# Optimization experiments

Measured on AMD Instinct MI355X. Metric: run time of the kernel, lower is better.

Reference implementation:

```python
import jax, jax.numpy as jnp
import numpy as np

B, T, N, C, K = 32, 16, 512, 128, 2


def setup_inputs() -> dict:
    key = jax.random.key(0)
    k1, k2, k3 = jax.random.split(key, 3)
    x = jax.random.normal(k1, (B, T, N, C), dtype=jnp.float32)
    adj = jax.random.uniform(k2, (B, N, N), dtype=jnp.float32)
    lambdas = jnp.ones((K,), dtype=jnp.float32)           # raw lambda params (init 1.0)
    thetas = jax.random.uniform(k3, (K, C, C), dtype=jnp.float32)  # torch.rand init
    return {"x": x, "adj": adj, "lambdas": lambdas, "thetas": thetas}


def _akgcn_layer(x, adj, lam_raw, theta):
    # x: [B,T,N,C], adj: [B,N,N]
    lam = 1.0 + jax.nn.relu(lam_raw)  # actual lambda
    h = jnp.einsum('btnc,cd->btnd', x, theta)
    eye = jnp.eye(adj.shape[-1], dtype=adj.dtype)
    v = ((2.0 * lam - 2.0) / lam) * eye + (2.0 / lam) * adj   # [B,N,N]
    v = v / jnp.sum(v, axis=-1, keepdims=True)                 # row-normalize
    out = jnp.einsum('bnm,btmd->btnd', v, h)                   # vectorized over T
    return jax.nn.relu(out)


def reference(x, adj, lambdas, thetas):
    hid = x
    for k in range(K):  # small fixed layer count
        hid = _akgcn_layer(hid, adj, lambdas[k], thetas[k])
    return jax.nn.relu(x) + jax.nn.sigmoid(hid)
```

## Files before the change

### kernel.cpp

```cpp
#include <hip/hip_runtime.h>
#include <hip/hip_bf16.h>

#define BB 32
#define TT 16
#define NNODE 512
#define CC 128

typedef __attribute__((ext_vector_type(8))) short bf16x8;
typedef __attribute__((ext_vector_type(4))) short short4_t;
typedef __attribute__((ext_vector_type(4))) float f32x4;

__device__ __forceinline__ short f2bf(float f) {
    __hip_bfloat16 h = __float2bfloat16(f);
    return *reinterpret_cast<short*>(&h);
}

#define GLD16(g, l)                                                          \
    __builtin_amdgcn_global_load_lds(                                        \
        (const __attribute__((address_space(1))) unsigned int*)(g),          \
        (__attribute__((address_space(3))) unsigned int*)(l), 16, 0, 0)

__global__ void prep_adj_kernel(const float* __restrict__ adj,
                                const float* __restrict__ lambdas, int layer0,
                                short* __restrict__ Abf0,
                                short* __restrict__ Abf1) {
    int gid = blockIdx.x * blockDim.x + threadIdx.x;
    int row = gid >> 6;
    int lane = gid & 63;
    int n = row & (NNODE - 1);
    const float* r = adj + (long)row * NNODE;
    float4 f0 = *(const float4*)(r + lane * 4);
    float4 f1 = *(const float4*)(r + 256 + lane * 4);
    float s = f0.x + f0.y + f0.z + f0.w + f1.x + f1.y + f1.z + f1.w;
#pragma unroll
    for (int o = 32; o; o >>= 1) s += __shfl_xor(s, o, 64);
    float base[8] = {f0.x, f0.y, f0.z, f0.w, f1.x, f1.y, f1.z, f1.w};
    int d0 = n - lane * 4;
    int d1 = n - 256 - lane * 4;
#pragma unroll
    for (int l = 0; l < 2; ++l) {
        short* dst = l ? Abf1 : Abf0;
        if (dst == nullptr) continue;
        float lamm1 = fmaxf(lambdas[layer0 + l], 0.f);
        float inv = 1.f / (s + lamm1);
        float v[8];
#pragma unroll
        for (int j = 0; j < 8; ++j) v[j] = base[j] * inv;
        if (d0 >= 0 && d0 < 4) v[d0] += lamm1 * inv;
        if (d1 >= 0 && d1 < 4) v[4 + d1] += lamm1 * inv;
        short* o = dst + (long)row * NNODE;
        short4_t s0 = {f2bf(v[0]), f2bf(v[1]), f2bf(v[2]), f2bf(v[3])};
        short4_t s1 = {f2bf(v[4]), f2bf(v[5]), f2bf(v[6]), f2bf(v[7])};
        *(short4_t*)(o + lane * 4) = s0;
        *(short4_t*)(o + 256 + lane * 4) = s1;
    }
}

__global__ void prep_theta_kernel(const float* __restrict__ thetas,
                                  short* __restrict__ thT) {
    int idx = blockIdx.x * 256 + threadIdx.x;
    int l = idx >> 14;
    int r = idx & 16383;
    int i = r >> 7, k = r & (CC - 1);
    thT[l * CC * CC + i * CC + k] = f2bf(thetas[l * CC * CC + k * CC + i]);
}

__global__ __launch_bounds__(256) void gemm_theta_mfma(
    const float* __restrict__ X, const short* __restrict__ thT,
    short* __restrict__ Ht) {
    __shared__ short Bs[128][136];
    const int t = threadIdx.x;
    const long rowBase = (long)blockIdx.x * 128;
    const int w = t >> 6, ln = t & 63;
    const int lm = ln & 15, q = ln >> 4;
    const int wy = w >> 1, wx = w & 1;

    {
        int row = t >> 1, half = (t & 1) * 64;
        const short* src = thT + row * CC + half;
#pragma unroll
        for (int j = 0; j < 8; ++j)
            *(bf16x8*)(&Bs[row][half + j * 8]) = *(const bf16x8*)(src + j * 8);
    }
    __syncthreads();

    f32x4 acc[4][4] = {};
    const float* Xr = X + (rowBase + wy * 64 + lm) * CC;
#pragma unroll
    for (int k0 = 0; k0 < CC; k0 += 32) {
        bf16x8 a[4], b[4];
#pragma unroll
        for (int i = 0; i < 4; ++i) {
            const float* p = Xr + i * 16 * CC + k0 + q * 8;
            float4 g0 = *(const float4*)(p);
            float4 g1 = *(const float4*)(p + 4);
            bf16x8 av;
            av[0] = f2bf(g0.x); av[1] = f2bf(g0.y);
            av[2] = f2bf(g0.z); av[3] = f2bf(g0.w);
            av[4] = f2bf(g1.x); av[5] = f2bf(g1.y);
            av[6] = f2bf(g1.z); av[7] = f2bf(g1.w);
            a[i] = av;
        }
#pragma unroll
        for (int j = 0; j < 4; ++j)
            b[j] = *(const bf16x8*)(&Bs[wx * 64 + j * 16 + lm][k0 + q * 8]);
#pragma unroll
        for (int i = 0; i < 4; ++i)
#pragma unroll
            for (int j = 0; j < 4; ++j)
                acc[i][j] = __builtin_amdgcn_mfma_f32_16x16x32_bf16(
                    a[i], b[j], acc[i][j], 0, 0, 0);
    }

    const long bt = rowBase >> 9;
    const int mBase = (int)(rowBase & (NNODE - 1));
    short* Hb = Ht + bt * (long)(NNODE * CC);
#pragma unroll
    for (int i = 0; i < 4; ++i) {
        int m = mBase + wy * 64 + i * 16 + q * 4;
#pragma unroll
        for (int j = 0; j < 4; ++j) {
            int c = wx * 64 + j * 16 + lm;
            f32x4 v = acc[i][j];
            short4_t sv = {f2bf(v[0]), f2bf(v[1]), f2bf(v[2]), f2bf(v[3])};
            *(short4_t*)(&Hb[(long)c * NNODE + m]) = sv;
        }
    }
}

__global__ __launch_bounds__(256) void gemm_agg_theta(
    const short* __restrict__ Abf, const short* __restrict__ Ht1,
    const short* __restrict__ thT2, short* __restrict__ Ht2) {
    __shared__ short sh[17408];
    const int t = threadIdx.x;
    const int bid = blockIdx.x;
    const int wid = (bid & 7) * 256 + (bid >> 3);
    const int bt = wid >> 2;
    const int n0 = (wid & 3) * 128;
    const short* Ab = Abf + (long)(bt >> 4) * NNODE * NNODE + (long)n0 * NNODE;
    const short* Hb = Ht1 + (long)bt * NNODE * CC;
    const int w = t >> 6, ln = t & 63;
    const int lm = ln & 15, q = ln >> 4;
    const int wy = w >> 1, wx = w & 1;

    f32x4 acc[4][4] = {};

    const int rr = w * 32 + (ln >> 2);
    const int kc = (ln & 3) * 8;
    const short* ga = Ab + (long)rr * NNODE + kc;
    const short* gb = Hb + (long)rr * NNODE + kc;
    const int lofs = w * 1024 + ln * 8;

    GLD16(ga, sh + lofs);
    GLD16(ga + 16 * NNODE, sh + lofs + 512);
    GLD16(gb, sh + 8192 + lofs);
    GLD16(gb + 16 * NNODE, sh + 8192 + lofs + 512);
    __syncthreads();
    int sel = 0;
    for (int k0 = 0; k0 < NNODE; k0 += 32) {
        if (k0 + 32 < NNODE) {
            const int no = (sel ^ 1) * 4096 + lofs;
            GLD16(ga + k0 + 32, sh + no);
            GLD16(ga + k0 + 32 + 16 * NNODE, sh + no + 512);
            GLD16(gb + k0 + 32, sh + 8192 + no);
            GLD16(gb + k0 + 32 + 16 * NNODE, sh + 8192 + no + 512);
        }
        const short* Ac = sh + sel * 4096;
        const short* Bc = sh + 8192 + sel * 4096;
        bf16x8 a[4], b[4];
#pragma unroll
        for (int i = 0; i < 4; ++i)
            a[i] = *(const bf16x8*)(Ac + (wy * 64 + i * 16 + lm) * 32 + q * 8);
#pragma unroll
        for (int j = 0; j < 4; ++j)
            b[j] = *(const bf16x8*)(Bc + (wx * 64 + j * 16 + lm) * 32 + q * 8);
#pragma unroll
        for (int i = 0; i < 4; ++i)
#pragma unroll
            for (int j = 0; j < 4; ++j)
                acc[i][j] = __builtin_amdgcn_mfma_f32_16x16x32_bf16(
                    a[i], b[j], acc[i][j], 0, 0, 0);
        __syncthreads();
        sel ^= 1;
    }

    short(*Ts)[136] = (short(*)[136])sh;
#pragma unroll
    for (int i = 0; i < 4; ++i)
#pragma unroll
        for (int j = 0; j < 4; ++j)
#pragma unroll
            for (int r2 = 0; r2 < 4; ++r2)
                Ts[wy * 64 + i * 16 + q * 4 + r2][wx * 64 + j * 16 + lm] =
                    f2bf(fmaxf(acc[i][j][r2], 0.f));
    __syncthreads();

    f32x4 acc2[4][4] = {};
#pragma unroll
    for (int c0 = 0; c0 < CC; c0 += 32) {
        bf16x8 a[4], b[4];
#pragma unroll
        for (int i = 0; i < 4; ++i)
            a[i] = *(const bf16x8*)(&Ts[wy * 64 + i * 16 + lm][c0 + q * 8]);
#pragma unroll
        for (int j = 0; j < 4; ++j)
            b[j] = *(const bf16x8*)(thT2 + (wx * 64 + j * 16 + lm) * CC + c0 +
                                    q * 8);
#pragma unroll
        for (int i = 0; i < 4; ++i)
#pragma unroll
            for (int j = 0; j < 4; ++j)
                acc2[i][j] = __builtin_amdgcn_mfma_f32_16x16x32_bf16(
                    a[i], b[j], acc2[i][j], 0, 0, 0);
    }

    short* Hb2 = Ht2 + (long)bt * NNODE * CC;
#pragma unroll
    for (int i = 0; i < 4; ++i) {
        int m = n0 + wy * 64 + i * 16 + q * 4;
#pragma unroll
        for (int j = 0; j < 4; ++j) {
            int c = wx * 64 + j * 16 + lm;
            f32x4 v = acc2[i][j];
            short4_t sv = {f2bf(v[0]), f2bf(v[1]), f2bf(v[2]), f2bf(v[3])};
            *(short4_t*)(&Hb2[(long)c * NNODE + m]) = sv;
        }
    }
}

__global__ __launch_bounds__(256) void gemm_agg_mfma(
    const short* __restrict__ Abf, const short* __restrict__ Ht,
    const float* __restrict__ x, float* __restrict__ Out) {
    __shared__ short sh[16384];
    const int t = threadIdx.x;
    const int bid = blockIdx.x;
    const int wid = (bid & 7) * 256 + (bid >> 3);
    const int bt = wid >> 2;
    const int n0 = (wid & 3) * 128;
    const short* Ab = Abf + (long)(bt >> 4) * NNODE * NNODE + (long)n0 * NNODE;
    const short* Hb = Ht + (long)bt * NNODE * CC;
    const int w = t >> 6, ln = t & 63;
    const int lm = ln & 15, q = ln >> 4;
    const int wy = w >> 1, wx = w & 1;

    f32x4 acc[4][4] = {};

    const int rr = w * 32 + (ln >> 2);
    const int kc = (ln & 3) * 8;
    const short* ga = Ab + (long)rr * NNODE + kc;
    const short* gb = Hb + (long)rr * NNODE + kc;
    const int lofs = w * 1024 + ln * 8;

    GLD16(ga, sh + lofs);
    GLD16(ga + 16 * NNODE, sh + lofs + 512);
    GLD16(gb, sh + 8192 + lofs);
    GLD16(gb + 16 * NNODE, sh + 8192 + lofs + 512);
    __syncthreads();
    int sel = 0;
    for (int k0 = 0; k0 < NNODE; k0 += 32) {
        if (k0 + 32 < NNODE) {
            const int no = (sel ^ 1) * 4096 + lofs;
            GLD16(ga + k0 + 32, sh + no);
            GLD16(ga + k0 + 32 + 16 * NNODE, sh + no + 512);
            GLD16(gb + k0 + 32, sh + 8192 + no);
            GLD16(gb + k0 + 32 + 16 * NNODE, sh + 8192 + no + 512);
        }
        const short* Ac = sh + sel * 4096;
        const short* Bc = sh + 8192 + sel * 4096;
        bf16x8 a[4], b[4];
#pragma unroll
        for (int i = 0; i < 4; ++i)
            a[i] = *(const bf16x8*)(Ac + (wy * 64 + i * 16 + lm) * 32 + q * 8);
#pragma unroll
        for (int j = 0; j < 4; ++j)
            b[j] = *(const bf16x8*)(Bc + (wx * 64 + j * 16 + lm) * 32 + q * 8);
#pragma unroll
        for (int i = 0; i < 4; ++i)
#pragma unroll
            for (int j = 0; j < 4; ++j)
                acc[i][j] = __builtin_amdgcn_mfma_f32_16x16x32_bf16(
                    a[i], b[j], acc[i][j], 0, 0, 0);
        __syncthreads();
        sel ^= 1;
    }

    const long obase = (long)bt * NNODE * CC;
#pragma unroll
    for (int i = 0; i < 4; ++i) {
        int n = n0 + wy * 64 + i * 16 + q * 4;
#pragma unroll
        for (int j = 0; j < 4; ++j) {
            int c = wx * 64 + j * 16 + lm;
#pragma unroll
            for (int r2 = 0; r2 < 4; ++r2) {
                long idx = obase + (long)(n + r2) * CC + c;
                float v = fmaxf(acc[i][j][r2], 0.f);
                Out[idx] = fmaxf(x[idx], 0.f) + 1.f / (1.f + __expf(-v));
            }
        }
    }
}

extern "C" void kernel_launch(void* const* d_in, const int* in_sizes, int n_in,
                              void* d_out, int out_size, void* d_ws,
                              size_t ws_size, hipStream_t stream) {
    const float* x = (const float*)d_in[0];
    const float* adj = (const float*)d_in[1];
    const float* lambdas = (const float*)d_in[2];
    const float* thetas = (const float*)d_in[3];
    float* out = (float*)d_out;

    const long abf_elems = (long)BB * NNODE * NNODE;
    const long ht_elems = (long)BB * TT * NNODE * CC;
    const bool two =
        ws_size >= (size_t)(2 * abf_elems + ht_elems + 2 * CC * CC) * 2;

    short* Abf0 = (short*)d_ws;
    short* Abf1 = two ? Abf0 + abf_elems : Abf0;
    short* Ht2 = Abf1 + abf_elems;
    short* thT0 = Ht2 + ht_elems;
    short* thT1 = thT0 + CC * CC;
    short* Ht1 = (short*)out;

    dim3 blk(256);

    if (two) {
        prep_adj_kernel<<<4096, blk, 0, stream>>>(adj, lambdas, 0, Abf0, Abf1);
        prep_theta_kernel<<<128, blk, 0, stream>>>(thetas, thT0);
        gemm_theta_mfma<<<2048, blk, 0, stream>>>(x, thT0, Ht1);
        gemm_agg_theta<<<2048, blk, 0, stream>>>(Abf0, Ht1, thT1, Ht2);
        gemm_agg_mfma<<<2048, blk, 0, stream>>>(Abf1, Ht2, x, out);
    } else {
        prep_adj_kernel<<<4096, blk, 0, stream>>>(adj, lambdas, 0, Abf0,
                                                  nullptr);
        prep_theta_kernel<<<128, blk, 0, stream>>>(thetas, thT0);
        gemm_theta_mfma<<<2048, blk, 0, stream>>>(x, thT0, Ht1);
        gemm_agg_theta<<<2048, blk, 0, stream>>>(Abf0, Ht1, thT1, Ht2);
        prep_adj_kernel<<<4096, blk, 0, stream>>>(adj, lambdas, 1, Abf0,
                                                  nullptr);
        gemm_agg_mfma<<<2048, blk, 0, stream>>>(Abf0, Ht2, x, out);
    }
}
```

Measured before the change: 504.0 us.

## Replace double-buffered LDS pipeline with single-buffer loads and 2D grid

Drops the double-buffered LDS prefetch in both aggregation GEMMs and uses a single buffer with a sync before and after each tile load. It also replaces the XCD-swizzled 1D block index with a plain 2D grid. In the theta stage, theta is now staged through LDS via global_load_lds instead of being read straight from global memory. This simplifies the code and lowers LDS use, but it gives up the overlap of loads with MFMA and the L2 locality the swizzle provided.

```diff
diff --git a/kernel.cpp b/kernel.cpp
--- a/kernel.cpp
+++ b/kernel.cpp
@@ -131,12 +131,12 @@
 __global__ __launch_bounds__(256) void gemm_agg_theta(
     const short* __restrict__ Abf, const short* __restrict__ Ht1,
     const short* __restrict__ thT2, short* __restrict__ Ht2) {
-    __shared__ short sh[17408];
+    __shared__ short As[128 * 32];
+    __shared__ short Bs[128 * 32];
+    __shared__ short Ts[128][136];
     const int t = threadIdx.x;
-    const int bid = blockIdx.x;
-    const int wid = (bid & 7) * 256 + (bid >> 3);
-    const int bt = wid >> 2;
-    const int n0 = (wid & 3) * 128;
+    const int bt = blockIdx.y;
+    const int n0 = blockIdx.x * 128;
     const short* Ab = Abf + (long)(bt >> 4) * NNODE * NNODE + (long)n0 * NNODE;
     const short* Hb = Ht1 + (long)bt * NNODE * CC;
     const int w = t >> 6, ln = t & 63;
@@ -147,44 +147,34 @@
 
     const int rr = w * 32 + (ln >> 2);
     const int kc = (ln & 3) * 8;
-    const short* ga = Ab + (long)rr * NNODE + kc;
-    const short* gb = Hb + (long)rr * NNODE + kc;
-    const int lofs = w * 1024 + ln * 8;
-
-    GLD16(ga, sh + lofs);
-    GLD16(ga + 16 * NNODE, sh + lofs + 512);
-    GLD16(gb, sh + 8192 + lofs);
-    GLD16(gb + 16 * NNODE, sh + 8192 + lofs + 512);
-    __syncthreads();
-    int sel = 0;
+    short* ldsA = As + w * 1024 + ln * 8;
+    short* ldsB = Bs + w * 1024 + ln * 8;
+
     for (int k0 = 0; k0 < NNODE; k0 += 32) {
-        if (k0 + 32 < NNODE) {
-            const int no = (sel ^ 1) * 4096 + lofs;
-            GLD16(ga + k0 + 32, sh + no);
-            GLD16(ga + k0 + 32 + 16 * NNODE, sh + no + 512);
-            GLD16(gb + k0 + 32, sh + 8192 + no);
-            GLD16(gb + k0 + 32 + 16 * NNODE, sh + 8192 + no + 512);
-        }
-        const short* Ac = sh + sel * 4096;
-        const short* Bc = sh + 8192 + sel * 4096;
+        __syncthreads();
+        const short* ga = Ab + (long)rr * NNODE + k0 + kc;
+        const short* gb = Hb + (long)rr * NNODE + k0 + kc;
+        GLD16(ga, ldsA);
+        GLD16(ga + 16 * NNODE, ldsA + 512);
+        GLD16(gb, ldsB);
+        GLD16(gb + 16 * NNODE, ldsB + 512);
+        __syncthreads();
+
         bf16x8 a[4], b[4];
 #pragma unroll
         for (int i = 0; i < 4; ++i)
-            a[i] = *(const bf16x8*)(Ac + (wy * 64 + i * 16 + lm) * 32 + q * 8);
-#pragma unroll
-        for (int j = 0; j < 4; ++j)
-            b[j] = *(const bf16x8*)(Bc + (wx * 64 + j * 16 + lm) * 32 + q * 8);
+            a[i] = *(const bf16x8*)(&As[(wy * 64 + i * 16 + lm) * 32 + q * 8]);
+#pragma unroll
+        for (int j = 0; j < 4; ++j)
+            b[j] = *(const bf16x8*)(&Bs[(wx * 64 + j * 16 + lm) * 32 + q * 8]);
 #pragma unroll
         for (int i = 0; i < 4; ++i)
 #pragma unroll
             for (int j = 0; j < 4; ++j)
                 acc[i][j] = __builtin_amdgcn_mfma_f32_16x16x32_bf16(
                     a[i], b[j], acc[i][j], 0, 0, 0);
-        __syncthreads();
-        sel ^= 1;
-    }
-
-    short(*Ts)[136] = (short(*)[136])sh;
+    }
+
 #pragma unroll
     for (int i = 0; i < 4; ++i)
 #pragma unroll
@@ -193,19 +183,22 @@
             for (int r2 = 0; r2 < 4; ++r2)
                 Ts[wy * 64 + i * 16 + q * 4 + r2][wx * 64 + j * 16 + lm] =
                     f2bf(fmaxf(acc[i][j][r2], 0.f));
-    __syncthreads();
 
     f32x4 acc2[4][4] = {};
-#pragma unroll
     for (int c0 = 0; c0 < CC; c0 += 32) {
+        __syncthreads();
+        const short* gb = thT2 + rr * CC + c0 + kc;
+        GLD16(gb, ldsB);
+        GLD16(gb + 16 * CC, ldsB + 512);
+        __syncthreads();
+
         bf16x8 a[4], b[4];
 #pragma unroll
         for (int i = 0; i < 4; ++i)
             a[i] = *(const bf16x8*)(&Ts[wy * 64 + i * 16 + lm][c0 + q * 8]);
 #pragma unroll
         for (int j = 0; j < 4; ++j)
-            b[j] = *(const bf16x8*)(thT2 + (wx * 64 + j * 16 + lm) * CC + c0 +
-                                    q * 8);
+            b[j] = *(const bf16x8*)(&Bs[(wx * 64 + j * 16 + lm) * 32 + q * 8]);
 #pragma unroll
         for (int i = 0; i < 4; ++i)
 #pragma unroll
@@ -231,12 +224,11 @@
 __global__ __launch_bounds__(256) void gemm_agg_mfma(
     const short* __restrict__ Abf, const short* __restrict__ Ht,
     const float* __restrict__ x, float* __restrict__ Out) {
-    __shared__ short sh[16384];
+    __shared__ short As[128 * 32];
+    __shared__ short Bs[128 * 32];
     const int t = threadIdx.x;
-    const int bid = blockIdx.x;
-    const int wid = (bid & 7) * 256 + (bid >> 3);
-    const int bt = wid >> 2;
-    const int n0 = (wid & 3) * 128;
+    const int bt = blockIdx.y;
+    const int n0 = blockIdx.x * 128;
     const short* Ab = Abf + (long)(bt >> 4) * NNODE * NNODE + (long)n0 * NNODE;
     const short* Hb = Ht + (long)bt * NNODE * CC;
     const int w = t >> 6, ln = t & 63;
@@ -247,41 +239,32 @@
 
     const int rr = w * 32 + (ln >> 2);
     const int kc = (ln & 3) * 8;
-    const short* ga = Ab + (long)rr * NNODE + kc;
-    const short* gb = Hb + (long)rr * NNODE + kc;
-    const int lofs = w * 1024 + ln * 8;
-
-    GLD16(ga, sh + lofs);
-    GLD16(ga + 16 * NNODE, sh + lofs + 512);
-    GLD16(gb, sh + 8192 + lofs);
-    GLD16(gb + 16 * NNODE, sh + 8192 + lofs + 512);
-    __syncthreads();
-    int sel = 0;
+    short* ldsA = As + w * 1024 + ln * 8;
+    short* ldsB = Bs + w * 1024 + ln * 8;
+
     for (int k0 = 0; k0 < NNODE; k0 += 32) {
-        if (k0 + 32 < NNODE) {
-            const int no = (sel ^ 1) * 4096 + lofs;
-            GLD16(ga + k0 + 32, sh + no);
-            GLD16(ga + k0 + 32 + 16 * NNODE, sh + no + 512);
-            GLD16(gb + k0 + 32, sh + 8192 + no);
-            GLD16(gb + k0 + 32 + 16 * NNODE, sh + 8192 + no + 512);
-        }
-        const short* Ac = sh + sel * 4096;
-        const short* Bc = sh + 8192 + sel * 4096;
+        __syncthreads();
+        const short* ga = Ab + (long)rr * NNODE + k0 + kc;
+        const short* gb = Hb + (long)rr * NNODE + k0 + kc;
+        GLD16(ga, ldsA);
+        GLD16(ga + 16 * NNODE, ldsA + 512);
+        GLD16(gb, ldsB);
+        GLD16(gb + 16 * NNODE, ldsB + 512);
+        __syncthreads();
+
         bf16x8 a[4], b[4];
 #pragma unroll
         for (int i = 0; i < 4; ++i)
-            a[i] = *(const bf16x8*)(Ac + (wy * 64 + i * 16 + lm) * 32 + q * 8);
-#pragma unroll
-        for (int j = 0; j < 4; ++j)
-            b[j] = *(const bf16x8*)(Bc + (wx * 64 + j * 16 + lm) * 32 + q * 8);
+            a[i] = *(const bf16x8*)(&As[(wy * 64 + i * 16 + lm) * 32 + q * 8]);
+#pragma unroll
+        for (int j = 0; j < 4; ++j)
+            b[j] = *(const bf16x8*)(&Bs[(wx * 64 + j * 16 + lm) * 32 + q * 8]);
 #pragma unroll
         for (int i = 0; i < 4; ++i)
 #pragma unroll
             for (int j = 0; j < 4; ++j)
                 acc[i][j] = __builtin_amdgcn_mfma_f32_16x16x32_bf16(
                     a[i], b[j], acc[i][j], 0, 0, 0);
-        __syncthreads();
-        sel ^= 1;
     }
 
     const long obase = (long)bt * NNODE * CC;
@@ -323,21 +306,22 @@
     short* Ht1 = (short*)out;
 
     dim3 blk(256);
+    dim3 g_agg(NNODE / 128, BB * TT);
 
     if (two) {
         prep_adj_kernel<<<4096, blk, 0, stream>>>(adj, lambdas, 0, Abf0, Abf1);
         prep_theta_kernel<<<128, blk, 0, stream>>>(thetas, thT0);
         gemm_theta_mfma<<<2048, blk, 0, stream>>>(x, thT0, Ht1);
-        gemm_agg_theta<<<2048, blk, 0, stream>>>(Abf0, Ht1, thT1, Ht2);
-        gemm_agg_mfma<<<2048, blk, 0, stream>>>(Abf1, Ht2, x, out);
+        gemm_agg_theta<<<g_agg, blk, 0, stream>>>(Abf0, Ht1, thT1, Ht2);
+        gemm_agg_mfma<<<g_agg, blk, 0, stream>>>(Abf1, Ht2, x, out);
     } else {
         prep_adj_kernel<<<4096, blk, 0, stream>>>(adj, lambdas, 0, Abf0,
                                                   nullptr);
         prep_theta_kernel<<<128, blk, 0, stream>>>(thetas, thT0);
         gemm_theta_mfma<<<2048, blk, 0, stream>>>(x, thT0, Ht1);
-        gemm_agg_theta<<<2048, blk, 0, stream>>>(Abf0, Ht1, thT1, Ht2);
+        gemm_agg_theta<<<g_agg, blk, 0, stream>>>(Abf0, Ht1, thT1, Ht2);
         prep_adj_kernel<<<4096, blk, 0, stream>>>(adj, lambdas, 1, Abf0,
                                                   nullptr);
-        gemm_agg_mfma<<<2048, blk, 0, stream>>>(Abf0, Ht2, x, out);
-    }
-}
+        gemm_agg_mfma<<<g_agg, blk, 0, stream>>>(Abf0, Ht2, x, out);
+    }
+}
```

Result: faster. 445.1 us (-11.7%).

## Overlap next-tile loads with compute via partial vmcnt waits and 2D grid

Applied to the files above, without the earlier changes.

The two aggregation GEMM kernels now issue the next K-tile's global-to-LDS loads and then wait only for the previous tile (vmcnt(4)) before a raw s_barrier, instead of a full __syncthreads that drains all outstanding loads. This lets the prefetch actually overlap the MFMA work. The block index mapping also changes from an XCD-swizzled 1D grid to a plain 2D grid (node tile, batch*time), which alters which blocks share adjacency tiles in cache. There is a risk that the mapping change hurts L2 locality across XCDs, and that the hand-written waitcnt is fragile if the compiler reorders loads.

```diff
diff --git a/kernel.cpp b/kernel.cpp
--- a/kernel.cpp
+++ b/kernel.cpp
@@ -133,10 +133,8 @@
     const short* __restrict__ thT2, short* __restrict__ Ht2) {
     __shared__ short sh[17408];
     const int t = threadIdx.x;
-    const int bid = blockIdx.x;
-    const int wid = (bid & 7) * 256 + (bid >> 3);
-    const int bt = wid >> 2;
-    const int n0 = (wid & 3) * 128;
+    const int bt = blockIdx.y;
+    const int n0 = blockIdx.x * 128;
     const short* Ab = Abf + (long)(bt >> 4) * NNODE * NNODE + (long)n0 * NNODE;
     const short* Hb = Ht1 + (long)bt * NNODE * CC;
     const int w = t >> 6, ln = t & 63;
@@ -155,7 +153,7 @@
     GLD16(ga + 16 * NNODE, sh + lofs + 512);
     GLD16(gb, sh + 8192 + lofs);
     GLD16(gb + 16 * NNODE, sh + 8192 + lofs + 512);
-    __syncthreads();
+
     int sel = 0;
     for (int k0 = 0; k0 < NNODE; k0 += 32) {
         if (k0 + 32 < NNODE) {
@@ -164,7 +162,11 @@
             GLD16(ga + k0 + 32 + 16 * NNODE, sh + no + 512);
             GLD16(gb + k0 + 32, sh + 8192 + no);
             GLD16(gb + k0 + 32 + 16 * NNODE, sh + 8192 + no + 512);
-        }
+            asm volatile("s_waitcnt vmcnt(4)" ::: "memory");
+        } else {
+            asm volatile("s_waitcnt vmcnt(0)" ::: "memory");
+        }
+        __builtin_amdgcn_s_barrier();
         const short* Ac = sh + sel * 4096;
         const short* Bc = sh + 8192 + sel * 4096;
         bf16x8 a[4], b[4];
@@ -180,7 +182,8 @@
             for (int j = 0; j < 4; ++j)
                 acc[i][j] = __builtin_amdgcn_mfma_f32_16x16x32_bf16(
                     a[i], b[j], acc[i][j], 0, 0, 0);
-        __syncthreads();
+        asm volatile("" ::: "memory");
+        __builtin_amdgcn_s_barrier();
         sel ^= 1;
     }
 
@@ -231,12 +234,11 @@
 __global__ __launch_bounds__(256) void gemm_agg_mfma(
     const short* __restrict__ Abf, const short* __restrict__ Ht,
     const float* __restrict__ x, float* __restrict__ Out) {
-    __shared__ short sh[16384];
+    __shared__ short As[2][4096];
+    __shared__ short Bs[2][4096];
     const int t = threadIdx.x;
-    const int bid = blockIdx.x;
-    const int wid = (bid & 7) * 256 + (bid >> 3);
-    const int bt = wid >> 2;
-    const int n0 = (wid & 3) * 128;
+    const int bt = blockIdx.y;
+    const int n0 = blockIdx.x * 128;
     const short* Ab = Abf + (long)(bt >> 4) * NNODE * NNODE + (long)n0 * NNODE;
     const short* Hb = Ht + (long)bt * NNODE * CC;
     const int w = t >> 6, ln = t & 63;
@@ -251,22 +253,25 @@
     const short* gb = Hb + (long)rr * NNODE + kc;
     const int lofs = w * 1024 + ln * 8;
 
-    GLD16(ga, sh + lofs);
-    GLD16(ga + 16 * NNODE, sh + lofs + 512);
-    GLD16(gb, sh + 8192 + lofs);
-    GLD16(gb + 16 * NNODE, sh + 8192 + lofs + 512);
-    __syncthreads();
+    GLD16(ga, &As[0][lofs]);
+    GLD16(ga + 16 * NNODE, &As[0][lofs + 512]);
+    GLD16(gb, &Bs[0][lofs]);
+    GLD16(gb + 16 * NNODE, &Bs[0][lofs + 512]);
+
     int sel = 0;
     for (int k0 = 0; k0 < NNODE; k0 += 32) {
         if (k0 + 32 < NNODE) {
-            const int no = (sel ^ 1) * 4096 + lofs;
-            GLD16(ga + k0 + 32, sh + no);
-            GLD16(ga + k0 + 32 + 16 * NNODE, sh + no + 512);
-            GLD16(gb + k0 + 32, sh + 8192 + no);
-            GLD16(gb + k0 + 32 + 16 * NNODE, sh + 8192 + no + 512);
-        }
-        const short* Ac = sh + sel * 4096;
-        const short* Bc = sh + 8192 + sel * 4096;
+            GLD16(ga + k0 + 32, &As[sel ^ 1][lofs]);
+            GLD16(ga + k0 + 32 + 16 * NNODE, &As[sel ^ 1][lofs + 512]);
+            GLD16(gb + k0 + 32, &Bs[sel ^ 1][lofs]);
+            GLD16(gb + k0 + 32 + 16 * NNODE, &Bs[sel ^ 1][lofs + 512]);
+            asm volatile("s_waitcnt vmcnt(4)" ::: "memory");
+        } else {
+            asm volatile("s_waitcnt vmcnt(0)" ::: "memory");
+        }
+        __builtin_amdgcn_s_barrier();
+        const short* Ac = As[sel];
+        const short* Bc = Bs[sel];
         bf16x8 a[4], b[4];
 #pragma unroll
         for (int i = 0; i < 4; ++i)
@@ -280,7 +285,8 @@
             for (int j = 0; j < 4; ++j)
                 acc[i][j] = __builtin_amdgcn_mfma_f32_16x16x32_bf16(
                     a[i], b[j], acc[i][j], 0, 0, 0);
-        __syncthreads();
+        asm volatile("" ::: "memory");
+        __builtin_amdgcn_s_barrier();
         sel ^= 1;
     }
 
@@ -323,21 +329,22 @@
     short* Ht1 = (short*)out;
 
     dim3 blk(256);
+    dim3 g_agg(NNODE / 128, BB * TT);
 
     if (two) {
         prep_adj_kernel<<<4096, blk, 0, stream>>>(adj, lambdas, 0, Abf0, Abf1);
         prep_theta_kernel<<<128, blk, 0, stream>>>(thetas, thT0);
         gemm_theta_mfma<<<2048, blk, 0, stream>>>(x, thT0, Ht1);
-        gemm_agg_theta<<<2048, blk, 0, stream>>>(Abf0, Ht1, thT1, Ht2);
-        gemm_agg_mfma<<<2048, blk, 0, stream>>>(Abf1, Ht2, x, out);
+        gemm_agg_theta<<<g_agg, blk, 0, stream>>>(Abf0, Ht1, thT1, Ht2);
+        gemm_agg_mfma<<<g_agg, blk, 0, stream>>>(Abf1, Ht2, x, out);
     } else {
         prep_adj_kernel<<<4096, blk, 0, stream>>>(adj, lambdas, 0, Abf0,
                                                   nullptr);
         prep_theta_kernel<<<128, blk, 0, stream>>>(thetas, thT0);
         gemm_theta_mfma<<<2048, blk, 0, stream>>>(x, thT0, Ht1);
-        gemm_agg_theta<<<2048, blk, 0, stream>>>(Abf0, Ht1, thT1, Ht2);
+        gemm_agg_theta<<<g_agg, blk, 0, stream>>>(Abf0, Ht1, thT1, Ht2);
         prep_adj_kernel<<<4096, blk, 0, stream>>>(adj, lambdas, 1, Abf0,
                                                   nullptr);
-        gemm_agg_mfma<<<2048, blk, 0, stream>>>(Abf0, Ht2, x, out);
-    }
-}
+        gemm_agg_mfma<<<g_agg, blk, 0, stream>>>(Abf0, Ht2, x, out);
+    }
+}
```

Result: no change. 500.7 us (-0.7%).
